# Performance work log

Measured on AMD Instinct MI355X. Metric: run time of the kernel, lower is better.

The kernel has to match this reference:

```python
import jax, jax.numpy as jnp
import numpy as np

EMBED_DIM = 1536
NUM_HEADS = 12
HEAD_DIM = EMBED_DIM // NUM_HEADS  # 128
SEQ = 2048
EPS = 1e-5


def rms_norm(x, w):
    # x: (..., HEAD_DIM)
    var = jnp.mean(jnp.square(x), axis=-1, keepdims=True)
    return x * jax.lax.rsqrt(var + EPS) * w


def apply_rotary(x, cos, sin):
    # x: (b, s, h, d); cos/sin: (s, d/2) -> broadcast (1, s, 1, d/2)
    d2 = cos.shape[-1]
    c = cos[None, :, None, :]
    s_ = sin[None, :, None, :]
    x1, x2 = x[..., :d2], x[..., d2:]
    return jnp.concatenate([x1 * c - x2 * s_, x2 * c + x1 * s_], axis=-1)


def setup_inputs() -> dict:
    key = jax.random.key(0)
    ks = jax.random.split(key, 10)
    x = jax.random.normal(ks[0], (SEQ, 1, EMBED_DIM), dtype=jnp.float32)
    cu_seqlens = jnp.array([0, SEQ // 2, SEQ], dtype=jnp.int32)
    # rotary tables for positions 0..SEQ-1, rotary dim = HEAD_DIM
    inv_freq = 1.0 / (10000.0 ** (jnp.arange(0, HEAD_DIM, 2, dtype=jnp.float32) / HEAD_DIM))
    pos = jnp.arange(SEQ, dtype=jnp.float32)
    freqs = pos[:, None] * inv_freq[None, :]  # (s, d/2)
    rotary_pos_emb_cos = jnp.cos(freqs)
    rotary_pos_emb_sin = jnp.sin(freqs)
    scale = 0.02
    w_qkv = jax.random.normal(ks[1], (EMBED_DIM, 3 * EMBED_DIM), dtype=jnp.float32) * scale
    b_qkv = jnp.zeros((3 * EMBED_DIM,), dtype=jnp.float32)
    q_norm_w = jnp.ones((HEAD_DIM,), dtype=jnp.float32)
    k_norm_w = jnp.ones((HEAD_DIM,), dtype=jnp.float32)
    w_proj = jax.random.normal(ks[2], (EMBED_DIM, EMBED_DIM), dtype=jnp.float32) * scale
    b_proj = jnp.zeros((EMBED_DIM,), dtype=jnp.float32)
    return {
        'x': x, 'cu_seqlens': cu_seqlens,
        'rotary_pos_emb_cos': rotary_pos_emb_cos, 'rotary_pos_emb_sin': rotary_pos_emb_sin,
        'w_qkv': w_qkv, 'b_qkv': b_qkv, 'q_norm_w': q_norm_w, 'k_norm_w': k_norm_w,
        'w_proj': w_proj, 'b_proj': b_proj,
    }


def reference(x, cu_seqlens, rotary_pos_emb_cos, rotary_pos_emb_sin,
              w_qkv, b_qkv, q_norm_w, k_norm_w, w_proj, b_proj):
    s, b, e = x.shape
    h, d = NUM_HEADS, HEAD_DIM
    qkv = jnp.einsum('sbe,ef->sbf', x, w_qkv) + b_qkv  # (s, b, 3e)
    q, k, v = jnp.split(qkv, 3, axis=2)
    q = q.reshape(s, b, h, d)
    k = k.reshape(s, b, h, d)
    v = v.reshape(s, b, h, d)
    # per-head RMSNorm on q/k
    q = rms_norm(q, q_norm_w)
    k = rms_norm(k, k_norm_w)
    # (s, b, h, d) -> (b, s, h, d)
    q = jnp.transpose(q, (1, 0, 2, 3))
    k = jnp.transpose(k, (1, 0, 2, 3))
    v = jnp.transpose(v, (1, 0, 2, 3))
    q = apply_rotary(q, rotary_pos_emb_cos, rotary_pos_emb_sin)
    k = apply_rotary(k, rotary_pos_emb_cos, rotary_pos_emb_sin)
    # varlen (block-diagonal, non-causal) attention via segment mask
    pos = jnp.arange(s)
    seg = jnp.searchsorted(cu_seqlens[1:], pos, side='right')  # (s,)
    mask = seg[:, None] == seg[None, :]  # (s, s)
    scale = d ** -0.5
    scores = jnp.einsum('bqhd,bkhd->bhqk', q, k) * scale  # (b, h, s, s)
    scores = jnp.where(mask[None, None, :, :], scores, jnp.finfo(scores.dtype).min)
    attn = jax.nn.softmax(scores, axis=-1)
    ctx = jnp.einsum('bhqk,bkhd->bqhd', attn, v)  # (b, s, h, d)
    # (b, s, h, d) -> (s, b, h*d)
    ctx = jnp.transpose(ctx, (1, 0, 2, 3)).reshape(s, b, h * d)
    out = jnp.einsum('sbe,ef->sbf', ctx, w_proj) + b_proj
    return out
```

## Files before the change

### kernel.cpp

```cpp
#include <hip/hip_runtime.h>
#include <hip/hip_bf16.h>
#include <stdint.h>

#define S_LEN 2048
#define EMB   1536
#define NH    12
#define HD    128
#define N3    4608
#define RMS_EPS 1e-5f
#define ATTN_SCALE 0.08838834764831845f
#define SPLIT 2
#define LOG2E 1.44269504088896f
#define DEFER_THR 11.5416f

typedef short short8_t __attribute__((ext_vector_type(8)));
typedef float f32x4    __attribute__((ext_vector_type(4)));

typedef __attribute__((address_space(1))) const void g1_void;
typedef __attribute__((address_space(3))) void l3_void;

__device__ __forceinline__ void gload_lds16(const void* g, void* l) {
  __builtin_amdgcn_global_load_lds((g1_void*)g, (l3_void*)l, 16, 0, 0);
}

__device__ __forceinline__ short f2bf(float f) {
  union { float f; unsigned u; } v; v.f = f;
  unsigned r = (v.u + 0x7FFFu + ((v.u >> 16) & 1u)) >> 16;
  return (short)(r & 0xFFFFu);
}
__device__ __forceinline__ float bf2f(short s) {
  union { unsigned u; float f; } v; v.u = ((unsigned)(unsigned short)s) << 16;
  return v.f;
}

__global__ __launch_bounds__(256) void k_cvt_bf16(const float* __restrict__ in,
                                                  short* __restrict__ out, int n) {
  int i = (blockIdx.x * 256 + threadIdx.x) * 4;
  if (i + 3 < n) {
    float4 v = *(const float4*)(in + i);
    short4 o;
    o.x = f2bf(v.x); o.y = f2bf(v.y); o.z = f2bf(v.z); o.w = f2bf(v.w);
    *(short4*)(out + i) = o;
  }
}

__global__ __launch_bounds__(256) void k_transpose_cvt(const float* __restrict__ W,
                                                       short* __restrict__ Wt,
                                                       int K, int N) {
  __shared__ float t[32][33];
  int n0 = blockIdx.x * 32, k0 = blockIdx.y * 32;
  int tx = threadIdx.x, ty = threadIdx.y;
#pragma unroll
  for (int r = 0; r < 4; ++r) {
    int k = ty + r * 8;
    t[k][tx] = W[(size_t)(k0 + k) * N + n0 + tx];
  }
  __syncthreads();
#pragma unroll
  for (int r = 0; r < 4; ++r) {
    int j = ty + r * 8;
    Wt[(size_t)(n0 + j) * K + k0 + tx] = f2bf(t[tx][j]);
  }
}

template<bool OBF>
__global__ __launch_bounds__(256, 2) void k_gemm_v4(const short* __restrict__ A,
                                                    const short* __restrict__ Bt,
                                                    const float* __restrict__ bias,
                                                    void* __restrict__ Cv,
                                                    int M, int N, int K) {
  __shared__ short lds[2][2][128 * 64];
  const int tid = threadIdx.x;
  const int lane = tid & 63, wid = tid >> 6;
  const int wr = (wid >> 1) * 64, wc = (wid & 1) * 64;
  const int bn = blockIdx.x * 128, bm = blockIdx.y * 128;
  const int lr = lane & 15, lg = lane >> 4;
  const int swz = (lr & 7) << 4;

  const int srow = lane >> 3;
  const int skc  = ((lane & 7) ^ srow) * 8;

  f32x4 acc[4][4] = {};
  const int nk = K >> 6;

#define GSTAGE(kt_, buf_)                                                          \
  {                                                                                \
    const int kt__ = (kt_);                                                        \
    _Pragma("unroll")                                                              \
    for (int it = 0; it < 4; ++it) {                                               \
      int seg = wid * 4 + it;                                                      \
      int row = seg * 8 + srow;                                                    \
      gload_lds16(A  + (size_t)(bm + row) * K + kt__ + skc, &lds[buf_][0][seg * 512]); \
      gload_lds16(Bt + (size_t)(bn + row) * K + kt__ + skc, &lds[buf_][1][seg * 512]); \
    }                                                                              \
  }

  GSTAGE(0, 0);
  if (nk > 1) {
    GSTAGE(64, 1);
    asm volatile("s_waitcnt vmcnt(8)" ::: "memory");
  } else {
    asm volatile("s_waitcnt vmcnt(0)" ::: "memory");
  }
  __builtin_amdgcn_s_barrier();

  int cur = 0;
  for (int t = 0; t < nk; ++t) {
    const char* baseA = (const char*)&lds[cur][0][0];
    const char* baseB = (const char*)&lds[cur][1][0];
    __builtin_amdgcn_s_setprio(1);
#pragma unroll
    for (int kk = 0; kk < 2; ++kk) {
      short8_t af[4], bfr[4];
#pragma unroll
      for (int m = 0; m < 4; ++m) {
        int row = wr + m * 16 + lr;
        af[m] = *(const short8_t*)(baseA + ((row * 128 + kk * 64 + lg * 16) ^ swz));
      }
#pragma unroll
      for (int n = 0; n < 4; ++n) {
        int row = wc + n * 16 + lr;
        bfr[n] = *(const short8_t*)(baseB + ((row * 128 + kk * 64 + lg * 16) ^ swz));
      }
#pragma unroll
      for (int m = 0; m < 4; ++m)
#pragma unroll
        for (int n = 0; n < 4; ++n)
          acc[m][n] = __builtin_amdgcn_mfma_f32_16x16x32_bf16(af[m], bfr[n], acc[m][n], 0, 0, 0);
    }
    __builtin_amdgcn_s_setprio(0);

    __builtin_amdgcn_s_barrier();
    if (t + 2 < nk) {
      GSTAGE((t + 2) << 6, cur);
      asm volatile("s_waitcnt vmcnt(8)" ::: "memory");
    } else {
      asm volatile("s_waitcnt vmcnt(0)" ::: "memory");
    }
    __builtin_amdgcn_s_barrier();
    cur ^= 1;
  }
#undef GSTAGE

#pragma unroll
  for (int m = 0; m < 4; ++m)
#pragma unroll
    for (int n = 0; n < 4; ++n) {
      int col = bn + wc + n * 16 + lr;
      float bv = bias[col];
#pragma unroll
      for (int r = 0; r < 4; ++r) {
        int row = bm + wr + m * 16 + lg * 4 + r;
        float v = acc[m][n][r] + bv;
        if (OBF) ((short*)Cv)[(size_t)row * N + col] = f2bf(v);
        else     ((float*)Cv)[(size_t)row * N + col] = v;
      }
    }
}

__global__ __launch_bounds__(256) void k_post(const short* __restrict__ qkv,
                                              const float* __restrict__ cosv,
                                              const float* __restrict__ sinv,
                                              const float* __restrict__ qw,
                                              const float* __restrict__ kw,
                                              short* __restrict__ qb,
                                              short* __restrict__ kb,
                                              short* __restrict__ vt) {
  __shared__ short ldsv[64 * 130];
  const int h = blockIdx.x, s0 = blockIdx.y * 64;
  const int t = threadIdx.x;
  const int r = t >> 2, j = t & 3;
  const int s = s0 + r;
  const size_t rowbase = (size_t)s * N3 + h * HD;
  const float SC2 = ATTN_SCALE * LOG2E;

  {
    const short* vp = qkv + rowbase + 2 * EMB + j * 32;
#pragma unroll
    for (int i4 = 0; i4 < 4; ++i4)
      *(short8_t*)&ldsv[r * 130 + j * 32 + i4 * 8] = *(const short8_t*)(vp + i4 * 8);
  }

#pragma unroll
  for (int qk = 0; qk < 2; ++qk) {
    const short* p = qkv + rowbase + qk * EMB + j * 32;
    const float* w = qk ? kw : qw;
    float v[32];
#pragma unroll
    for (int i4 = 0; i4 < 4; ++i4) {
      short8_t x = *(const short8_t*)(p + i4 * 8);
#pragma unroll
      for (int e = 0; e < 8; ++e) v[i4 * 8 + e] = bf2f(x[e]);
    }
    float ss = 0.f;
#pragma unroll
    for (int i = 0; i < 32; ++i) ss += v[i] * v[i];
    ss += __shfl_xor(ss, 1);
    ss += __shfl_xor(ss, 2);
    float rsq = rsqrtf(ss * (1.0f / HD) + RMS_EPS);
    if (qk == 0) rsq *= SC2;
#pragma unroll
    for (int i = 0; i < 32; ++i) v[i] = v[i] * rsq * w[j * 32 + i];
    const float* cp = cosv + (size_t)s * 64 + (j & 1) * 32;
    const float* sp = sinv + (size_t)s * 64 + (j & 1) * 32;
    short out[32];
#pragma unroll
    for (int i = 0; i < 32; ++i) {
      float part = __shfl_xor(v[i], 2);
      float c = cp[i], sn = sp[i];
      float o = (j < 2) ? (v[i] * c - part * sn) : (v[i] * c + part * sn);
      out[i] = f2bf(o);
    }
    short* dst = (qk ? kb : qb) + ((size_t)h * S_LEN + s) * HD + j * 32;
#pragma unroll
    for (int i4 = 0; i4 < 4; ++i4) {
      short8_t o8;
#pragma unroll
      for (int e = 0; e < 8; ++e) o8[e] = out[i4 * 8 + e];
      *(short8_t*)(dst + i4 * 8) = o8;
    }
  }

  __syncthreads();
  const int sl = t & 63, wv = t >> 6;
#pragma unroll
  for (int it = 0; it < 32; ++it) {
    int d = it * 4 + wv;
    vt[((size_t)h * HD + d) * S_LEN + s0 + sl] = ldsv[sl * 130 + d];
  }
}

__global__ __launch_bounds__(512, 2) void k_attn(const short* __restrict__ qb,
                                                 const short* __restrict__ kb,
                                                 const short* __restrict__ vt,
                                                 const int* __restrict__ cu, int nseg,
                                                 short* __restrict__ Opart,
                                                 float* __restrict__ mlpart) {
  __shared__ short ldsK[2][8192];
  __shared__ short ldsV[2][128 * 64];
  __shared__ short ldsP[8 * 16 * 64];

  const int wg = blockIdx.x;
  const int member = wg / 48;
  const int c = wg % 48;
  const int p = c & 1;
  const int h = c >> 2;
  const int qt = ((c >> 1) & 1) * 8 + member;

  const int q0 = qt * 128;
  const int tid = threadIdx.x, l = tid & 63, w = tid >> 6;
  const int lr = l & 15, lg = l >> 4;

  const short* kb_h = kb + (size_t)h * S_LEN * HD;
  const short* vt_h = vt + (size_t)h * HD * S_LEN;

  const int qrow_sm = q0 + w * 16 + lr;
  int segq = 0;
  for (int i = 1; i <= nseg; ++i) if (qrow_sm >= cu[i]) segq = i;
  const int rs_s = (segq == 0) ? 0 : cu[segq];
  const int re_s = (segq < nseg) ? cu[segq + 1] : S_LEN;
  float m = -INFINITY, lsum = 0.f;

  int seg0 = 0, seg1 = 0;
  for (int i = 1; i <= nseg; ++i) {
    if (q0 >= cu[i]) seg0 = i;
    if (q0 + 127 >= cu[i]) seg1 = i;
  }
  const int ks = (seg0 == 0) ? 0 : cu[seg0];
  const int ke = (seg1 < nseg) ? cu[seg1 + 1] : S_LEN;
  const int kt0 = (ks >> 6) << 6;
  const int nt = (ke - kt0 + 63) >> 6;
  const int tpb = (nt + SPLIT - 1) / SPLIT;
  const int tb0 = p * tpb;
  const int tb1 = (tb0 + tpb < nt) ? tb0 + tpb : nt;

  const int vseg_row = l >> 3;

  short8_t qf[4];
  {
    int srow = q0 + w * 16 + lr;
    const short* qp = qb + ((size_t)h * S_LEN + srow) * HD;
#pragma unroll
    for (int kk = 0; kk < 4; ++kk)
      qf[kk] = *(const short8_t*)(qp + kk * 32 + lg * 8);
  }

  f32x4 cacc[8] = {};

#define STAGE(kt_, buf_)                                                          \
  {                                                                               \
    const int kt__ = (kt_);                                                       \
    _Pragma("unroll")                                                             \
    for (int it = 0; it < 2; ++it) {                                              \
      int s = w * 2 + it;                                                         \
      int half = s >> 3;                                                          \
      int krow = (s & 7) * 8 + (l >> 3);                                          \
      int kc = half * 64 + (((l & 7) ^ (l >> 3)) * 8);                            \
      gload_lds16(kb_h + (size_t)(kt__ + krow) * HD + kc, &ldsK[buf_][s * 512]);  \
      int drow = s * 8 + vseg_row;                                                \
      int sv = ((l & 7) ^ (drow & 7)) * 8;                                        \
      gload_lds16(vt_h + (size_t)drow * S_LEN + kt__ + sv, &ldsV[buf_][s * 512]); \
    }                                                                             \
  }

  if (tb0 < tb1)     STAGE(kt0 + tb0 * 64, 0);
  if (tb0 + 1 < tb1) {
    STAGE(kt0 + (tb0 + 1) * 64, 1);
    asm volatile("s_waitcnt vmcnt(4)" ::: "memory");
  } else {
    asm volatile("s_waitcnt vmcnt(0)" ::: "memory");
  }
  __builtin_amdgcn_s_barrier();

  int cur = 0;
  for (int ti = tb0; ti < tb1; ++ti) {
    const int kt = kt0 + ti * 64;
    const char* bK = (const char*)&ldsK[cur][0];
    const char* bV = (const char*)&ldsV[cur][0];

    f32x4 sacc[4] = {};
    __builtin_amdgcn_s_setprio(1);
#pragma unroll
    for (int n = 0; n < 4; ++n) {
#pragma unroll
      for (int kk = 0; kk < 4; ++kk) {
        int row = n * 16 + lr;
        int byte = (kk >> 1) * 8192 + row * 128 + (kk & 1) * 64 + lg * 16;
        byte ^= (lr & 7) << 4;
        short8_t kf = *(const short8_t*)(bK + byte);
        sacc[n] = __builtin_amdgcn_mfma_f32_16x16x32_bf16(kf, qf[kk], sacc[n], 0, 0, 0);
      }
    }
    __builtin_amdgcn_s_setprio(0);

    if (!__all((kt >= rs_s) && (kt + 64 <= re_s))) {
#pragma unroll
      for (int n = 0; n < 4; ++n) {
        int kbase = kt + n * 16 + lg * 4;
#pragma unroll
        for (int r = 0; r < 4; ++r) {
          int key = kbase + r;
          sacc[n][r] = (key >= rs_s && key < re_s) ? sacc[n][r] : -1e30f;
        }
      }
    }

    float tm = sacc[0][0];
#pragma unroll
    for (int n = 0; n < 4; ++n)
#pragma unroll
      for (int r = 0; r < 4; ++r) tm = fmaxf(tm, sacc[n][r]);
    tm = fmaxf(tm, __shfl_xor(tm, 16));
    tm = fmaxf(tm, __shfl_xor(tm, 32));

    if (!__all(tm <= m + DEFER_THR)) {
      float mn = fmaxf(m, tm);
      float alpha = exp2f(m - mn);
      m = mn;
      lsum *= alpha;
      float a[4];
#pragma unroll
      for (int r = 0; r < 4; ++r) a[r] = __shfl(alpha, lg * 4 + r);
#pragma unroll
      for (int n = 0; n < 8; ++n)
#pragma unroll
        for (int r = 0; r < 4; ++r) cacc[n][r] *= a[r];
    }

    float ls = 0.f;
#pragma unroll
    for (int n = 0; n < 4; ++n) {
      short4 p4;
      float p0 = exp2f(sacc[n][0] - m);
      float p1 = exp2f(sacc[n][1] - m);
      float p2 = exp2f(sacc[n][2] - m);
      float p3 = exp2f(sacc[n][3] - m);
      ls += (p0 + p1) + (p2 + p3);
      p4.x = f2bf(p0); p4.y = f2bf(p1); p4.z = f2bf(p2); p4.w = f2bf(p3);
      int byte = lr * 128 + (n * 16 + lg * 4) * 2;
      byte ^= (lr & 7) << 4;
      *(short4*)((char*)ldsP + w * 2048 + byte) = p4;
    }
    ls += __shfl_xor(ls, 16);
    ls += __shfl_xor(ls, 32);
    lsum += ls;

    __builtin_amdgcn_s_setprio(1);
#pragma unroll
    for (int kk = 0; kk < 2; ++kk) {
      int byteP = lr * 128 + (kk * 32 + lg * 8) * 2;
      byteP ^= (lr & 7) << 4;
      short8_t pf = *(const short8_t*)((const char*)ldsP + w * 2048 + byteP);
#pragma unroll
      for (int n = 0; n < 8; ++n) {
        int d = n * 16 + lr;
        int byteV = d * 128 + (kk * 32 + lg * 8) * 2;
        byteV ^= (d & 7) << 4;
        short8_t vf = *(const short8_t*)(bV + byteV);
        cacc[n] = __builtin_amdgcn_mfma_f32_16x16x32_bf16(pf, vf, cacc[n], 0, 0, 0);
      }
    }
    __builtin_amdgcn_s_setprio(0);

    __builtin_amdgcn_s_barrier();
    if (ti + 2 < tb1) {
      STAGE(kt0 + (ti + 2) * 64, cur);
      asm volatile("s_waitcnt vmcnt(4)" ::: "memory");
    } else {
      asm volatile("s_waitcnt vmcnt(0)" ::: "memory");
    }
    __builtin_amdgcn_s_barrier();
    cur ^= 1;
  }
#undef STAGE

  const int b = (h * 16 + qt) * SPLIT + p;
#pragma unroll
  for (int r = 0; r < 4; ++r) {
    int qrow = w * 16 + lg * 4 + r;
#pragma unroll
    for (int n = 0; n < 8; ++n)
      Opart[(size_t)b * 16384 + qrow * 128 + n * 16 + lr] = f2bf(cacc[n][r]);
  }
  if (lg == 0) {
    mlpart[(size_t)b * 256 + w * 16 + lr] = m;
    mlpart[(size_t)b * 256 + 128 + w * 16 + lr] = lsum;
  }
}

__global__ __launch_bounds__(512) void k_combine(const short* __restrict__ Opart,
                                                 const float* __restrict__ ml,
                                                 short* __restrict__ ctx) {
  const int h = blockIdx.x, qt = blockIdx.y, t = threadIdx.x;
  const int r = t >> 2, j = t & 3;
  const int b0 = (h * 16 + qt) * SPLIT;

  float mp[SPLIT], lp[SPLIT], wp[SPLIT];
  float M = -INFINITY;
#pragma unroll
  for (int p = 0; p < SPLIT; ++p) {
    mp[p] = ml[(size_t)(b0 + p) * 256 + r];
    lp[p] = ml[(size_t)(b0 + p) * 256 + 128 + r];
    M = fmaxf(M, mp[p]);
  }
  float L = 0.f;
#pragma unroll
  for (int p = 0; p < SPLIT; ++p) {
    wp[p] = exp2f(mp[p] - M);
    L += lp[p] * wp[p];
  }
  const float inv = 1.0f / L;

  float acc[32];
#pragma unroll
  for (int i = 0; i < 32; ++i) acc[i] = 0.f;
#pragma unroll
  for (int p = 0; p < SPLIT; ++p) {
    const short* src = Opart + (size_t)(b0 + p) * 16384 + r * 128 + j * 32;
#pragma unroll
    for (int i4 = 0; i4 < 4; ++i4) {
      short8_t v = *(const short8_t*)(src + i4 * 8);
#pragma unroll
      for (int e = 0; e < 8; ++e) acc[i4 * 8 + e] += wp[p] * bf2f(v[e]);
    }
  }

  short* dst = ctx + (size_t)(qt * 128 + r) * EMB + h * HD + j * 32;
#pragma unroll
  for (int i4 = 0; i4 < 4; ++i4) {
    short8_t o8;
#pragma unroll
    for (int e = 0; e < 8; ++e) o8[e] = f2bf(acc[i4 * 8 + e] * inv);
    *(short8_t*)(dst + i4 * 8) = o8;
  }
}

extern "C" void kernel_launch(void* const* d_in, const int* in_sizes, int n_in,
                              void* d_out, int out_size, void* d_ws, size_t ws_size,
                              hipStream_t stream) {
  const float* x      = (const float*)d_in[0];
  const int*   cu     = (const int*)d_in[1];
  const float* cosv   = (const float*)d_in[2];
  const float* sinv   = (const float*)d_in[3];
  const float* w_qkv  = (const float*)d_in[4];
  const float* b_qkv  = (const float*)d_in[5];
  const float* q_norm = (const float*)d_in[6];
  const float* k_norm = (const float*)d_in[7];
  const float* w_proj = (const float*)d_in[8];
  const float* b_proj = (const float*)d_in[9];
  const int nseg = in_sizes[1] - 1;

  char* ws = (char*)d_ws;
  short* xb     = (short*)(ws);
  short* wqkvT  = (short*)(ws + 6291456);
  short* wprojT = (short*)(ws + 20447232);
  short* qkv16  = (short*)(ws + 25165824);
  short* qb     = (short*)(ws + 44040192);
  short* kb     = (short*)(ws + 50331648);
  short* vt     = (short*)(ws + 56623104);
  short* ctxb   = (short*)(ws + 62914560);
  short* Opart  = qkv16;
  float* mlpart = (float*)ws;

  k_cvt_bf16<<<(S_LEN * EMB) / 1024, 256, 0, stream>>>(x, xb, S_LEN * EMB);
  k_transpose_cvt<<<dim3(N3 / 32, EMB / 32), dim3(32, 8), 0, stream>>>(w_qkv, wqkvT, EMB, N3);
  k_transpose_cvt<<<dim3(EMB / 32, EMB / 32), dim3(32, 8), 0, stream>>>(w_proj, wprojT, EMB, EMB);
  k_gemm_v4<true><<<dim3(N3 / 128, S_LEN / 128), 256, 0, stream>>>(xb, wqkvT, b_qkv, qkv16, S_LEN, N3, EMB);
  k_post<<<dim3(NH, S_LEN / 64), 256, 0, stream>>>(qkv16, cosv, sinv, q_norm, k_norm, qb, kb, vt);
  k_attn<<<dim3(NH * (S_LEN / 128) * SPLIT), 512, 0, stream>>>(qb, kb, vt, cu, nseg, Opart, mlpart);
  k_combine<<<dim3(NH, S_LEN / 128), 512, 0, stream>>>(Opart, mlpart, ctxb);
  k_gemm_v4<false><<<dim3(EMB / 128, S_LEN / 128), 256, 0, stream>>>(ctxb, wprojT, b_proj, (float*)d_out, S_LEN, EMB, EMB);
}
```

Measured before the change: 132.0 us.

## Remap GEMM tiles across XCDs and issue next-stage loads before MFMAs

```diff
diff --git a/kernel.cpp b/kernel.cpp
--- a/kernel.cpp
+++ b/kernel.cpp
@@ -64,7 +64,7 @@
 }
 
 template<bool OBF>
-__global__ __launch_bounds__(256, 2) void k_gemm_v4(const short* __restrict__ A,
+__global__ __launch_bounds__(256, 2) void k_gemm_v5(const short* __restrict__ A,
                                                     const short* __restrict__ Bt,
                                                     const float* __restrict__ bias,
                                                     void* __restrict__ Cv,
@@ -73,10 +73,15 @@
   const int tid = threadIdx.x;
   const int lane = tid & 63, wid = tid >> 6;
   const int wr = (wid >> 1) * 64, wc = (wid & 1) * 64;
-  const int bn = blockIdx.x * 128, bm = blockIdx.y * 128;
+
+  const int nbn = N >> 7;
+  const int per = (nbn * (M >> 7)) >> 3;
+  const int logical = (blockIdx.x & 7) * per + (blockIdx.x >> 3);
+  const int bm = (logical / nbn) * 128;
+  const int bn = (logical % nbn) * 128;
+
   const int lr = lane & 15, lg = lane >> 4;
   const int swz = (lr & 7) << 4;
-
   const int srow = lane >> 3;
   const int skc  = ((lane & 7) ^ srow) * 8;
 
@@ -108,31 +113,34 @@
   for (int t = 0; t < nk; ++t) {
     const char* baseA = (const char*)&lds[cur][0][0];
     const char* baseB = (const char*)&lds[cur][1][0];
+
+    short8_t af[2][4], bfr[2][4];
+#pragma unroll
+    for (int kk = 0; kk < 2; ++kk)
+#pragma unroll
+      for (int m = 0; m < 4; ++m) {
+        int rowA = wr + m * 16 + lr;
+        af[kk][m]  = *(const short8_t*)(baseA + ((rowA * 128 + kk * 64 + lg * 16) ^ swz));
+        int rowB = wc + m * 16 + lr;
+        bfr[kk][m] = *(const short8_t*)(baseB + ((rowB * 128 + kk * 64 + lg * 16) ^ swz));
+      }
+    asm volatile("s_waitcnt lgkmcnt(0)" ::: "memory");
+    __builtin_amdgcn_sched_barrier(0);
+    __builtin_amdgcn_s_barrier();
+
+    if (t + 2 < nk) GSTAGE((t + 2) << 6, cur);
+
     __builtin_amdgcn_s_setprio(1);
 #pragma unroll
-    for (int kk = 0; kk < 2; ++kk) {
-      short8_t af[4], bfr[4];
-#pragma unroll
-      for (int m = 0; m < 4; ++m) {
-        int row = wr + m * 16 + lr;
-        af[m] = *(const short8_t*)(baseA + ((row * 128 + kk * 64 + lg * 16) ^ swz));
-      }
-#pragma unroll
-      for (int n = 0; n < 4; ++n) {
-        int row = wc + n * 16 + lr;
-        bfr[n] = *(const short8_t*)(baseB + ((row * 128 + kk * 64 + lg * 16) ^ swz));
-      }
+    for (int kk = 0; kk < 2; ++kk)
 #pragma unroll
       for (int m = 0; m < 4; ++m)
 #pragma unroll
         for (int n = 0; n < 4; ++n)
-          acc[m][n] = __builtin_amdgcn_mfma_f32_16x16x32_bf16(af[m], bfr[n], acc[m][n], 0, 0, 0);
-    }
+          acc[m][n] = __builtin_amdgcn_mfma_f32_16x16x32_bf16(af[kk][m], bfr[kk][n], acc[m][n], 0, 0, 0);
     __builtin_amdgcn_s_setprio(0);
 
-    __builtin_amdgcn_s_barrier();
     if (t + 2 < nk) {
-      GSTAGE((t + 2) << 6, cur);
       asm volatile("s_waitcnt vmcnt(8)" ::: "memory");
     } else {
       asm volatile("s_waitcnt vmcnt(0)" ::: "memory");
@@ -505,9 +513,9 @@
   k_cvt_bf16<<<(S_LEN * EMB) / 1024, 256, 0, stream>>>(x, xb, S_LEN * EMB);
   k_transpose_cvt<<<dim3(N3 / 32, EMB / 32), dim3(32, 8), 0, stream>>>(w_qkv, wqkvT, EMB, N3);
   k_transpose_cvt<<<dim3(EMB / 32, EMB / 32), dim3(32, 8), 0, stream>>>(w_proj, wprojT, EMB, EMB);
-  k_gemm_v4<true><<<dim3(N3 / 128, S_LEN / 128), 256, 0, stream>>>(xb, wqkvT, b_qkv, qkv16, S_LEN, N3, EMB);
+  k_gemm_v5<true><<<dim3((N3 / 128) * (S_LEN / 128)), 256, 0, stream>>>(xb, wqkvT, b_qkv, qkv16, S_LEN, N3, EMB);
   k_post<<<dim3(NH, S_LEN / 64), 256, 0, stream>>>(qkv16, cosv, sinv, q_norm, k_norm, qb, kb, vt);
   k_attn<<<dim3(NH * (S_LEN / 128) * SPLIT), 512, 0, stream>>>(qb, kb, vt, cu, nseg, Opart, mlpart);
   k_combine<<<dim3(NH, S_LEN / 128), 512, 0, stream>>>(Opart, mlpart, ctxb);
-  k_gemm_v4<false><<<dim3(EMB / 128, S_LEN / 128), 256, 0, stream>>>(ctxb, wprojT, b_proj, (float*)d_out, S_LEN, EMB, EMB);
-}
+  k_gemm_v5<false><<<dim3((EMB / 128) * (S_LEN / 128)), 256, 0, stream>>>(ctxb, wprojT, b_proj, (float*)d_out, S_LEN, EMB, EMB);
+}
```

After: 135.8 us. 2.9% more time.
